# Kernel tuning notes

Measured on AMD Instinct MI355X. Metric: run time of the kernel, lower is better.

Reference implementation:

```python
import jax, jax.numpy as jnp
import numpy as np

N = 100000   # nodes
E = 1600000  # edges
D = 128      # in_dim == hidden_dim (residual-friendly)
C = 47       # num_classes
EPS = 1e-5   # BatchNorm eps


def _glorot(key, shape):
    fan = shape[0] + shape[1]
    return jax.random.uniform(key, shape, jnp.float32, -1.0, 1.0) * np.sqrt(6.0 / fan)


def setup_inputs() -> dict:
    key = jax.random.key(0)
    ks = jax.random.split(key, 16)
    inp = {
        "x": jax.random.normal(ks[0], (N, D), jnp.float32),
        "edge_index": jax.random.randint(ks[1], (2, E), 0, N, jnp.int32),
    }
    # Per-layer SAGEConv params: lin_l (root, with bias) and lin_r (neighbor, no bias)
    for i, k in zip((1, 2, 3), (ks[2], ks[3], ks[4])):
        k1, k2 = jax.random.split(k)
        inp[f"Wl{i}"] = _glorot(k1, (D, D))
        inp[f"bl{i}"] = jnp.zeros((D,), jnp.float32)
        inp[f"Wr{i}"] = _glorot(k2, (D, D))
        inp[f"bn_g{i}"] = jnp.ones((D,), jnp.float32)
        inp[f"bn_b{i}"] = jnp.zeros((D,), jnp.float32)
    inp["lin_W"] = _glorot(ks[5], (C, D))
    inp["lin_b"] = jnp.zeros((C,), jnp.float32)
    return inp


def _sage_conv(x, src, dst, Wl, bl, Wr):
    # mean aggregation of source features at destination nodes
    msg = jax.ops.segment_sum(x[src], dst, num_segments=N)            # [N, D]
    cnt = jax.ops.segment_sum(jnp.ones((src.shape[0],), x.dtype), dst, num_segments=N)
    mean = msg / jnp.maximum(cnt, 1.0)[:, None]
    return x @ Wl.T + bl + mean @ Wr.T


def _batch_norm(h, g, b):
    mu = h.mean(axis=0)
    var = h.var(axis=0)
    return (h - mu) * jax.lax.rsqrt(var + EPS) * g + b


def reference(x, edge_index,
              Wl1, bl1, Wr1, bn_g1, bn_b1,
              Wl2, bl2, Wr2, bn_g2, bn_b2,
              Wl3, bl3, Wr3, bn_g3, bn_b3,
              lin_W, lin_b):
    src, dst = edge_index[0], edge_index[1]
    layers = [(Wl1, bl1, Wr1, bn_g1, bn_b1),
              (Wl2, bl2, Wr2, bn_g2, bn_b2),
              (Wl3, bl3, Wr3, bn_g3, bn_b3)]
    for Wl, bl, Wr, g, b in layers:
        h = _sage_conv(x, src, dst, Wl, bl, Wr)
        h = jax.nn.relu(_batch_norm(h, g, b))
        # dropout is identity in deterministic/eval reference
        x = x + h  # shapes always match since in_dim == hidden_dim
    return x @ lin_W.T + lin_b
```

## Files before the change

kernel.cpp:

```cpp
#include <hip/hip_runtime.h>

typedef __attribute__((ext_vector_type(8))) short short8;
typedef __attribute__((ext_vector_type(4))) float f32x4;
typedef __attribute__((ext_vector_type(2))) float f32x2;

constexpr int NN = 100000;
constexpr int EE = 1600000;
constexpr int DD = 128;
constexpr int CC = 47;
constexpr int NB = 391;
constexpr int BSLOT = 5120;
constexpr int GB = 782;

constexpr size_t OFF_XB   = 0;
constexpr size_t OFF_MB   = 25600000;
constexpr size_t OFF_HB   = 51200000;
constexpr size_t OFF_XQ   = 76800000;
constexpr size_t OFF_BIN  = 89600000;
constexpr size_t OFF_CSR  = 97607680;
constexpr size_t OFF_RP   = 104007680;
constexpr size_t OFF_CUR  = 104407808;
constexpr size_t OFF_BASE = 104409856;
constexpr size_t OFF_W    = 104411904;
constexpr size_t OFF_ST   = 104620800;
constexpr size_t OFF_PB   = 104621824;

static __device__ __forceinline__ float bf2f(unsigned short u) {
    return __uint_as_float(((unsigned)u) << 16);
}
static __device__ __forceinline__ unsigned short f2bf(float f) {
    unsigned u = __float_as_uint(f);
    unsigned r = (u + 0x7fffu + ((u >> 16) & 1u)) >> 16;
    return (unsigned short)r;
}
static __device__ __forceinline__ uint2 pack8_fp8(const float* f) {
    int w0 = 0, w1 = 0;
    w0 = __builtin_amdgcn_cvt_pk_fp8_f32(f[0], f[1], w0, false);
    w0 = __builtin_amdgcn_cvt_pk_fp8_f32(f[2], f[3], w0, true);
    w1 = __builtin_amdgcn_cvt_pk_fp8_f32(f[4], f[5], w1, false);
    w1 = __builtin_amdgcn_cvt_pk_fp8_f32(f[6], f[7], w1, true);
    return uint2{(unsigned)w0, (unsigned)w1};
}

__global__ void k_convw(const float* __restrict__ wl1, const float* __restrict__ wr1,
                        const float* __restrict__ wl2, const float* __restrict__ wr2,
                        const float* __restrict__ wl3, const float* __restrict__ wr3,
                        const float* __restrict__ lw, unsigned short* __restrict__ dst) {
    int id = blockIdx.x * 256 + threadIdx.x;
    if (id < 98304) {
        int L = id >> 15;
        int r = id & 32767;
        int mat = r >> 14;
        int t = r & 16383;
        int j = t & 7, lane = (t >> 3) & 63, ct = (t >> 9) & 7, ks = t >> 12;
        int row = ct * 16 + (lane & 15);
        int col = ks * 32 + ((lane >> 4) << 3) + j;
        const float* src = (L == 0) ? (mat ? wr1 : wl1)
                         : (L == 1) ? (mat ? wr2 : wl2)
                                    : (mat ? wr3 : wl3);
        dst[id] = f2bf(src[row * 128 + col]);
    } else if (id < 98304 + 6144) {
        int t = id - 98304;
        int j = t & 7, lane = (t >> 3) & 63, m = t >> 9;
        int ct = m % 3, ks = m / 3;
        int row = ct * 16 + (lane & 15);
        int col = ks * 32 + ((lane >> 4) << 3) + j;
        dst[id] = (row < CC) ? f2bf(lw[row * 128 + col]) : (unsigned short)0;
    }
}

__global__ void k_convx(const float* __restrict__ x, unsigned short* __restrict__ xb,
                        unsigned char* __restrict__ xq) {
    int i = (blockIdx.x * 256 + threadIdx.x) * 8;
    if (i >= NN * DD) return;
    float4 v1 = *(const float4*)(x + i);
    float4 v2 = *(const float4*)(x + i + 4);
    float f[8] = {v1.x, v1.y, v1.z, v1.w, v2.x, v2.y, v2.z, v2.w};
    short8 o;
    #pragma unroll
    for (int j = 0; j < 8; ++j) o[j] = (short)f2bf(f[j]);
    *(short8*)(xb + i) = o;
    *(uint2*)(xq + i) = pack8_fp8(f);
}

__global__ __launch_bounds__(256) void k_bin(const int* __restrict__ ei,
                                             int* __restrict__ cur, int* __restrict__ bin) {
    __shared__ int cnt[NB];
    int t = threadIdx.x;
    for (int b = t; b < NB; b += 256) cnt[b] = 0;
    __syncthreads();
    int start = blockIdx.x * 3125;
    for (int i = t; i < 3125; i += 256) {
        int d = ei[EE + start + i];
        atomicAdd(&cnt[d >> 8], 1);
    }
    __syncthreads();
    int c[2], b0[2];
    #pragma unroll
    for (int k = 0; k < 2; ++k) {
        int b = t + k * 256;
        if (b < NB) { c[k] = cnt[b]; b0[k] = (c[k] > 0) ? atomicAdd(&cur[b], c[k]) : 0; }
    }
    __syncthreads();
    #pragma unroll
    for (int k = 0; k < 2; ++k) {
        int b = t + k * 256;
        if (b < NB) cnt[b] = b0[k];
    }
    __syncthreads();
    for (int i = t; i < 3125; i += 256) {
        int s = ei[start + i];
        int d = ei[EE + start + i];
        int b = d >> 8;
        int p = atomicAdd(&cnt[b], 1);
        if (p < BSLOT) bin[b * BSLOT + p] = (s << 8) | (d & 255);
    }
}

__global__ void k_base(const int* __restrict__ cur, int* __restrict__ base, int* __restrict__ rp) {
    __shared__ int sd[512];
    int t = threadIdx.x;
    int v0 = (t < NB) ? cur[t] : 0;
    sd[t] = v0;
    __syncthreads();
    for (int off = 1; off < 512; off <<= 1) {
        int v = (t >= off) ? sd[t - off] : 0;
        __syncthreads();
        sd[t] += v;
        __syncthreads();
    }
    if (t < NB) base[t] = sd[t] - v0;
    if (t == NB - 1) rp[NN] = sd[t];
}

__global__ __launch_bounds__(256) void k_build(const int* __restrict__ cur, const int* __restrict__ base,
                                               int* __restrict__ rp, const int* __restrict__ bin,
                                               int* __restrict__ csr) {
    __shared__ int lcnt[256], lsc[256], lrun[256];
    int b = blockIdx.x, t = threadIdx.x;
    int n0 = b << 8;
    int nodes = NN - n0; if (nodes > 256) nodes = 256;
    int tot = cur[b]; if (tot > BSLOT) tot = BSLOT;
    int bb = base[b];
    lcnt[t] = 0;
    __syncthreads();
    const int* bsrc = bin + b * BSLOT;
    for (int i = t; i < tot; i += 256) atomicAdd(&lcnt[bsrc[i] & 255], 1);
    __syncthreads();
    int c = lcnt[t];
    lsc[t] = c;
    __syncthreads();
    for (int off = 1; off < 256; off <<= 1) {
        int v = (t >= off) ? lsc[t - off] : 0;
        __syncthreads();
        lsc[t] += v;
        __syncthreads();
    }
    int excl = lsc[t] - c;
    if (t < nodes) rp[n0 + t] = bb + excl;
    lrun[t] = bb + excl;
    __syncthreads();
    for (int i = t; i < tot; i += 256) {
        int v = bsrc[i];
        int p = atomicAdd(&lrun[v & 255], 1);
        csr[p] = (v >> 8) << 7;
    }
}

__global__ __launch_bounds__(256) void k_agg(const int* __restrict__ rp, const int* __restrict__ csr,
                                             const unsigned char* __restrict__ xq,
                                             unsigned short* __restrict__ mb) {
    int node = blockIdx.x * 4 + (threadIdx.x >> 6);
    if (node >= NN) return;
    int lane = threadIdx.x & 63;
    int g = lane >> 4;
    int cb = (lane & 15) << 3;
    int s0 = rp[node], s1 = rp[node + 1];
    int deg = s1 - s0;
    f32x2 acc0 = {0.f, 0.f}, acc1 = {0.f, 0.f}, acc2 = {0.f, 0.f}, acc3 = {0.f, 0.f};
    int nb = deg >> 4;
    int e = s0 + g;
    for (int k = 0; k < nb; ++k) {
        int i0 = csr[e];
        int i1 = csr[e + 4];
        int i2 = csr[e + 8];
        int i3 = csr[e + 12];
        uint2 v0 = *(const uint2*)(xq + i0 + cb);
        uint2 v1 = *(const uint2*)(xq + i1 + cb);
        uint2 v2 = *(const uint2*)(xq + i2 + cb);
        uint2 v3 = *(const uint2*)(xq + i3 + cb);
        acc0 += __builtin_amdgcn_cvt_pk_f32_fp8(v0.x, false);
        acc1 += __builtin_amdgcn_cvt_pk_f32_fp8(v0.x, true);
        acc2 += __builtin_amdgcn_cvt_pk_f32_fp8(v0.y, false);
        acc3 += __builtin_amdgcn_cvt_pk_f32_fp8(v0.y, true);
        acc0 += __builtin_amdgcn_cvt_pk_f32_fp8(v1.x, false);
        acc1 += __builtin_amdgcn_cvt_pk_f32_fp8(v1.x, true);
        acc2 += __builtin_amdgcn_cvt_pk_f32_fp8(v1.y, false);
        acc3 += __builtin_amdgcn_cvt_pk_f32_fp8(v1.y, true);
        acc0 += __builtin_amdgcn_cvt_pk_f32_fp8(v2.x, false);
        acc1 += __builtin_amdgcn_cvt_pk_f32_fp8(v2.x, true);
        acc2 += __builtin_amdgcn_cvt_pk_f32_fp8(v2.y, false);
        acc3 += __builtin_amdgcn_cvt_pk_f32_fp8(v2.y, true);
        acc0 += __builtin_amdgcn_cvt_pk_f32_fp8(v3.x, false);
        acc1 += __builtin_amdgcn_cvt_pk_f32_fp8(v3.x, true);
        acc2 += __builtin_amdgcn_cvt_pk_f32_fp8(v3.y, false);
        acc3 += __builtin_amdgcn_cvt_pk_f32_fp8(v3.y, true);
        e += 16;
    }
    for (; e < s1; e += 4) {
        int i0 = csr[e];
        uint2 v0 = *(const uint2*)(xq + i0 + cb);
        acc0 += __builtin_amdgcn_cvt_pk_f32_fp8(v0.x, false);
        acc1 += __builtin_amdgcn_cvt_pk_f32_fp8(v0.x, true);
        acc2 += __builtin_amdgcn_cvt_pk_f32_fp8(v0.y, false);
        acc3 += __builtin_amdgcn_cvt_pk_f32_fp8(v0.y, true);
    }
    float acc[8] = {acc0[0], acc0[1], acc1[0], acc1[1],
                    acc2[0], acc2[1], acc3[0], acc3[1]};
    #pragma unroll
    for (int j = 0; j < 8; ++j) {
        acc[j] += __shfl_xor(acc[j], 16);
        acc[j] += __shfl_xor(acc[j], 32);
    }
    if (g == 0) {
        float inv = 1.0f / (float)(deg > 1 ? deg : 1);
        short8 o;
        #pragma unroll
        for (int j = 0; j < 8; ++j) o[j] = (short)f2bf(acc[j] * inv);
        *(short8*)(mb + (size_t)node * 128 + cb) = o;
    }
}

__global__ __launch_bounds__(256, 4) void k_gemm(const unsigned short* __restrict__ xb,
                                                 const unsigned short* __restrict__ mb,
                                                 const unsigned short* __restrict__ wf,
                                                 const float* __restrict__ bias,
                                                 unsigned short* __restrict__ hb,
                                                 float* __restrict__ pbuf) {
    __shared__ unsigned short wsh[16384];
    __shared__ float rbuf[1024];
    int tid = threadIdx.x;
    int wave = tid >> 6, lane = tid & 63, q = lane >> 4, l15 = lane & 15;
    int rowbase = blockIdx.x * 128 + wave * 32;

    f32x4 acc[2][8];
    #pragma unroll
    for (int ct = 0; ct < 8; ++ct) {
        float bv = bias[ct * 16 + l15];
        f32x4 t = {bv, bv, bv, bv};
        acc[0][ct] = t; acc[1][ct] = t;
    }

    #pragma unroll
    for (int mat = 0; mat < 2; ++mat) {
        const unsigned short* src = mat ? mb : xb;
        const int4* wsrc = (const int4*)(wf + (mat << 14));
        if (mat) __syncthreads();
        #pragma unroll
        for (int i = 0; i < 8; ++i)
            ((int4*)wsh)[tid + i * 256] = wsrc[tid + i * 256];
        __syncthreads();
        #pragma unroll
        for (int ks = 0; ks < 4; ++ks) {
            short8 a[2];
            #pragma unroll
            for (int rt = 0; rt < 2; ++rt) {
                int row = rowbase + rt * 16 + l15;
                if (row < NN) a[rt] = *(const short8*)(src + (size_t)row * 128 + ks * 32 + (q << 3));
                else          a[rt] = short8{0,0,0,0,0,0,0,0};
            }
            #pragma unroll
            for (int ct = 0; ct < 8; ++ct) {
                short8 b = *(const short8*)(wsh + ((ks * 8 + ct) << 9) + (lane << 3));
                acc[0][ct] = __builtin_amdgcn_mfma_f32_16x16x32_bf16(a[0], b, acc[0][ct], 0, 0, 0);
                acc[1][ct] = __builtin_amdgcn_mfma_f32_16x16x32_bf16(a[1], b, acc[1][ct], 0, 0, 0);
            }
        }
    }

    #pragma unroll
    for (int ct = 0; ct < 8; ++ct) {
        int colg = ct * 16 + l15;
        float sv = 0.f, qv = 0.f;
        #pragma unroll
        for (int rt = 0; rt < 2; ++rt) {
            #pragma unroll
            for (int r = 0; r < 4; ++r) {
                int row = rowbase + rt * 16 + (q << 2) + r;
                if (row < NN) {
                    float v = acc[rt][ct][r];
                    hb[(size_t)row * 128 + colg] = f2bf(v);
                    sv += v; qv += v * v;
                }
            }
        }
        sv += __shfl_xor(sv, 16); sv += __shfl_xor(sv, 32);
        qv += __shfl_xor(qv, 16); qv += __shfl_xor(qv, 32);
        if (q == 0) {
            rbuf[wave * 256 + colg] = sv;
            rbuf[wave * 256 + 128 + colg] = qv;
        }
    }
    __syncthreads();
    if (tid < 256) {
        float v = rbuf[tid] + rbuf[256 + tid] + rbuf[512 + tid] + rbuf[768 + tid];
        pbuf[(size_t)blockIdx.x * 256 + tid] = v;
    }
}

__global__ void k_stat2(const float* __restrict__ pbuf, float* __restrict__ st) {
    __shared__ float red[256];
    int b = blockIdx.x, t = threadIdx.x;
    int col = b * 32 + (t & 31);
    int rchunk = t >> 5;
    float s = 0.f;
    for (int r = rchunk; r < GB; r += 8) s += pbuf[(size_t)r * 256 + col];
    red[t] = s;
    __syncthreads();
    if (t < 32) {
        float v = 0.f;
        #pragma unroll
        for (int k = 0; k < 8; ++k) v += red[k * 32 + t];
        st[col] = v;
    }
}

__global__ void k_bn(const unsigned short* __restrict__ hb,
                     const float* __restrict__ stats, const float* __restrict__ gam,
                     const float* __restrict__ bet, unsigned short* __restrict__ xb,
                     unsigned char* __restrict__ xq) {
    int i = (blockIdx.x * 256 + threadIdx.x) * 8;
    if (i >= NN * DD) return;
    int col = i & 127;
    const float invN = 1.0f / (float)NN;
    short8 hv = *(const short8*)(hb + i);
    short8 xv = *(const short8*)(xb + i);
    short8 o;
    float f[8];
    #pragma unroll
    for (int j = 0; j < 8; ++j) {
        int c = col + j;
        float mu = stats[c] * invN;
        float var = stats[128 + c] * invN - mu * mu;
        float sc = rsqrtf(var + 1e-5f) * gam[c];
        float val = (bf2f((unsigned short)hv[j]) - mu) * sc + bet[c];
        float r = bf2f((unsigned short)xv[j]) + (val > 0.f ? val : 0.f);
        f[j] = r;
        o[j] = (short)f2bf(r);
    }
    *(short8*)(xb + i) = o;
    *(uint2*)(xq + i) = pack8_fp8(f);
}

__global__ __launch_bounds__(256) void k_final(const unsigned short* __restrict__ xb,
                                               const unsigned short* __restrict__ wf,
                                               const float* __restrict__ bias,
                                               float* __restrict__ out) {
    __shared__ unsigned short wsh[6144];
    int tid = threadIdx.x;
    #pragma unroll
    for (int i = 0; i < 3; ++i) {
        int idx = tid + i * 256;
        if (idx < 768) ((int4*)wsh)[idx] = ((const int4*)wf)[idx];
    }
    __syncthreads();

    int wave = tid >> 6, lane = tid & 63, q = lane >> 4, l15 = lane & 15;
    int rowbase = blockIdx.x * 256 + wave * 64;

    f32x4 acc[4][3];
    #pragma unroll
    for (int ct = 0; ct < 3; ++ct) {
        int colg = ct * 16 + l15;
        float bv = (colg < CC) ? bias[colg] : 0.f;
        f32x4 t = {bv, bv, bv, bv};
        #pragma unroll
        for (int rt = 0; rt < 4; ++rt) acc[rt][ct] = t;
    }
    #pragma unroll
    for (int ks = 0; ks < 4; ++ks) {
        short8 a[4];
        #pragma unroll
        for (int rt = 0; rt < 4; ++rt) {
            int row = rowbase + rt * 16 + l15;
            if (row < NN) a[rt] = *(const short8*)(xb + (size_t)row * 128 + ks * 32 + (q << 3));
            else          a[rt] = short8{0,0,0,0,0,0,0,0};
        }
        #pragma unroll
        for (int ct = 0; ct < 3; ++ct) {
            short8 b = *(const short8*)(wsh + ((ks * 3 + ct) << 9) + (lane << 3));
            #pragma unroll
            for (int rt = 0; rt < 4; ++rt)
                acc[rt][ct] = __builtin_amdgcn_mfma_f32_16x16x32_bf16(a[rt], b, acc[rt][ct], 0, 0, 0);
        }
    }
    #pragma unroll
    for (int ct = 0; ct < 3; ++ct) {
        int colg = ct * 16 + l15;
        if (colg >= CC) continue;
        #pragma unroll
        for (int rt = 0; rt < 4; ++rt) {
            #pragma unroll
            for (int r = 0; r < 4; ++r) {
                int row = rowbase + rt * 16 + (q << 2) + r;
                if (row < NN) out[(size_t)row * CC + colg] = acc[rt][ct][r];
            }
        }
    }
}

extern "C" void kernel_launch(void* const* d_in, const int* in_sizes, int n_in,
                              void* d_out, int out_size, void* d_ws, size_t ws_size,
                              hipStream_t stream) {
    const float* x   = (const float*)d_in[0];
    const int*   ei  = (const int*)d_in[1];
    const float* Wl[3]  = {(const float*)d_in[2],  (const float*)d_in[7],  (const float*)d_in[12]};
    const float* bl[3]  = {(const float*)d_in[3],  (const float*)d_in[8],  (const float*)d_in[13]};
    const float* Wr[3]  = {(const float*)d_in[4],  (const float*)d_in[9],  (const float*)d_in[14]};
    const float* bng[3] = {(const float*)d_in[5],  (const float*)d_in[10], (const float*)d_in[15]};
    const float* bnb[3] = {(const float*)d_in[6],  (const float*)d_in[11], (const float*)d_in[16]};
    const float* linW = (const float*)d_in[17];
    const float* linb = (const float*)d_in[18];

    char* ws = (char*)d_ws;
    unsigned short* xb   = (unsigned short*)(ws + OFF_XB);
    unsigned short* mb   = (unsigned short*)(ws + OFF_MB);
    unsigned short* hb   = (unsigned short*)(ws + OFF_HB);
    unsigned char*  xq   = (unsigned char*)(ws + OFF_XQ);
    int*            bin  = (int*)(ws + OFF_BIN);
    int*            csr  = (int*)(ws + OFF_CSR);
    int*            rp   = (int*)(ws + OFF_RP);
    int*            cur  = (int*)(ws + OFF_CUR);
    int*            base = (int*)(ws + OFF_BASE);
    unsigned short* wfr  = (unsigned short*)(ws + OFF_W);
    float*          st   = (float*)(ws + OFF_ST);
    float*          pbuf = (float*)(ws + OFF_PB);

    hipMemsetAsync(cur, 0, (size_t)NB * 4, stream);
    k_convw<<<408, 256, 0, stream>>>(Wl[0], Wr[0], Wl[1], Wr[1], Wl[2], Wr[2], linW, wfr);
    k_convx<<<6250, 256, 0, stream>>>(x, xb, xq);
    k_bin<<<512, 256, 0, stream>>>(ei, cur, bin);
    k_base<<<1, 512, 0, stream>>>(cur, base, rp);
    k_build<<<NB, 256, 0, stream>>>(cur, base, rp, bin, csr);

    for (int l = 0; l < 3; ++l) {
        k_agg<<<25000, 256, 0, stream>>>(rp, csr, xq, mb);
        k_gemm<<<GB, 256, 0, stream>>>(xb, mb, wfr + (size_t)l * 32768, bl[l], hb, pbuf);
        k_stat2<<<8, 256, 0, stream>>>(pbuf, st);
        k_bn<<<6250, 256, 0, stream>>>(hb, st, bng[l], bnb[l], xb, xq);
    }
    k_final<<<391, 256, 0, stream>>>(xb, wfr + 98304, linb, (float*)d_out);
}
```

Baseline: 532.2 us.

## Fuse neighbor aggregation into GEMM kernel via shared-memory mean tile

```diff
diff --git a/kernel.cpp b/kernel.cpp
--- a/kernel.cpp
+++ b/kernel.cpp
@@ -167,82 +167,84 @@
     }
 }
 
-__global__ __launch_bounds__(256) void k_agg(const int* __restrict__ rp, const int* __restrict__ csr,
-                                             const unsigned char* __restrict__ xq,
-                                             unsigned short* __restrict__ mb) {
-    int node = blockIdx.x * 4 + (threadIdx.x >> 6);
-    if (node >= NN) return;
-    int lane = threadIdx.x & 63;
-    int g = lane >> 4;
-    int cb = (lane & 15) << 3;
-    int s0 = rp[node], s1 = rp[node + 1];
-    int deg = s1 - s0;
-    f32x2 acc0 = {0.f, 0.f}, acc1 = {0.f, 0.f}, acc2 = {0.f, 0.f}, acc3 = {0.f, 0.f};
-    int nb = deg >> 4;
-    int e = s0 + g;
-    for (int k = 0; k < nb; ++k) {
-        int i0 = csr[e];
-        int i1 = csr[e + 4];
-        int i2 = csr[e + 8];
-        int i3 = csr[e + 12];
-        uint2 v0 = *(const uint2*)(xq + i0 + cb);
-        uint2 v1 = *(const uint2*)(xq + i1 + cb);
-        uint2 v2 = *(const uint2*)(xq + i2 + cb);
-        uint2 v3 = *(const uint2*)(xq + i3 + cb);
-        acc0 += __builtin_amdgcn_cvt_pk_f32_fp8(v0.x, false);
-        acc1 += __builtin_amdgcn_cvt_pk_f32_fp8(v0.x, true);
-        acc2 += __builtin_amdgcn_cvt_pk_f32_fp8(v0.y, false);
-        acc3 += __builtin_amdgcn_cvt_pk_f32_fp8(v0.y, true);
-        acc0 += __builtin_amdgcn_cvt_pk_f32_fp8(v1.x, false);
-        acc1 += __builtin_amdgcn_cvt_pk_f32_fp8(v1.x, true);
-        acc2 += __builtin_amdgcn_cvt_pk_f32_fp8(v1.y, false);
-        acc3 += __builtin_amdgcn_cvt_pk_f32_fp8(v1.y, true);
-        acc0 += __builtin_amdgcn_cvt_pk_f32_fp8(v2.x, false);
-        acc1 += __builtin_amdgcn_cvt_pk_f32_fp8(v2.x, true);
-        acc2 += __builtin_amdgcn_cvt_pk_f32_fp8(v2.y, false);
-        acc3 += __builtin_amdgcn_cvt_pk_f32_fp8(v2.y, true);
-        acc0 += __builtin_amdgcn_cvt_pk_f32_fp8(v3.x, false);
-        acc1 += __builtin_amdgcn_cvt_pk_f32_fp8(v3.x, true);
-        acc2 += __builtin_amdgcn_cvt_pk_f32_fp8(v3.y, false);
-        acc3 += __builtin_amdgcn_cvt_pk_f32_fp8(v3.y, true);
-        e += 16;
-    }
-    for (; e < s1; e += 4) {
-        int i0 = csr[e];
-        uint2 v0 = *(const uint2*)(xq + i0 + cb);
-        acc0 += __builtin_amdgcn_cvt_pk_f32_fp8(v0.x, false);
-        acc1 += __builtin_amdgcn_cvt_pk_f32_fp8(v0.x, true);
-        acc2 += __builtin_amdgcn_cvt_pk_f32_fp8(v0.y, false);
-        acc3 += __builtin_amdgcn_cvt_pk_f32_fp8(v0.y, true);
-    }
-    float acc[8] = {acc0[0], acc0[1], acc1[0], acc1[1],
-                    acc2[0], acc2[1], acc3[0], acc3[1]};
-    #pragma unroll
-    for (int j = 0; j < 8; ++j) {
-        acc[j] += __shfl_xor(acc[j], 16);
-        acc[j] += __shfl_xor(acc[j], 32);
-    }
-    if (g == 0) {
-        float inv = 1.0f / (float)(deg > 1 ? deg : 1);
-        short8 o;
-        #pragma unroll
-        for (int j = 0; j < 8; ++j) o[j] = (short)f2bf(acc[j] * inv);
-        *(short8*)(mb + (size_t)node * 128 + cb) = o;
-    }
-}
-
-__global__ __launch_bounds__(256, 4) void k_gemm(const unsigned short* __restrict__ xb,
-                                                 const unsigned short* __restrict__ mb,
-                                                 const unsigned short* __restrict__ wf,
-                                                 const float* __restrict__ bias,
-                                                 unsigned short* __restrict__ hb,
-                                                 float* __restrict__ pbuf) {
-    __shared__ unsigned short wsh[16384];
+__global__ __launch_bounds__(256, 4) void k_fused(const int* __restrict__ rp,
+                                                  const int* __restrict__ csr,
+                                                  const unsigned char* __restrict__ xq,
+                                                  const unsigned short* __restrict__ xb,
+                                                  const unsigned short* __restrict__ wf,
+                                                  const float* __restrict__ bias,
+                                                  unsigned short* __restrict__ hb,
+                                                  float* __restrict__ pbuf) {
+    __shared__ unsigned short msh[16384];
     __shared__ float rbuf[1024];
     int tid = threadIdx.x;
     int wave = tid >> 6, lane = tid & 63, q = lane >> 4, l15 = lane & 15;
     int rowbase = blockIdx.x * 128 + wave * 32;
 
+    int g = q;
+    int cb = l15 << 3;
+    #pragma unroll 1
+    for (int i = 0; i < 32; ++i) {
+        int node = rowbase + i;
+        if (node >= NN) break;
+        int s0 = rp[node], s1 = rp[node + 1];
+        int deg = s1 - s0;
+        f32x2 a0 = {0.f, 0.f}, a1 = {0.f, 0.f}, a2 = {0.f, 0.f}, a3 = {0.f, 0.f};
+        int nbt = deg >> 4;
+        int e = s0 + g;
+        for (int k = 0; k < nbt; ++k) {
+            int i0 = csr[e];
+            int i1 = csr[e + 4];
+            int i2 = csr[e + 8];
+            int i3 = csr[e + 12];
+            uint2 v0 = *(const uint2*)(xq + i0 + cb);
+            uint2 v1 = *(const uint2*)(xq + i1 + cb);
+            uint2 v2 = *(const uint2*)(xq + i2 + cb);
+            uint2 v3 = *(const uint2*)(xq + i3 + cb);
+            a0 += __builtin_amdgcn_cvt_pk_f32_fp8(v0.x, false);
+            a1 += __builtin_amdgcn_cvt_pk_f32_fp8(v0.x, true);
+            a2 += __builtin_amdgcn_cvt_pk_f32_fp8(v0.y, false);
+            a3 += __builtin_amdgcn_cvt_pk_f32_fp8(v0.y, true);
+            a0 += __builtin_amdgcn_cvt_pk_f32_fp8(v1.x, false);
+            a1 += __builtin_amdgcn_cvt_pk_f32_fp8(v1.x, true);
+            a2 += __builtin_amdgcn_cvt_pk_f32_fp8(v1.y, false);
+            a3 += __builtin_amdgcn_cvt_pk_f32_fp8(v1.y, true);
+            a0 += __builtin_amdgcn_cvt_pk_f32_fp8(v2.x, false);
+            a1 += __builtin_amdgcn_cvt_pk_f32_fp8(v2.x, true);
+            a2 += __builtin_amdgcn_cvt_pk_f32_fp8(v2.y, false);
+            a3 += __builtin_amdgcn_cvt_pk_f32_fp8(v2.y, true);
+            a0 += __builtin_amdgcn_cvt_pk_f32_fp8(v3.x, false);
+            a1 += __builtin_amdgcn_cvt_pk_f32_fp8(v3.x, true);
+            a2 += __builtin_amdgcn_cvt_pk_f32_fp8(v3.y, false);
+            a3 += __builtin_amdgcn_cvt_pk_f32_fp8(v3.y, true);
+            e += 16;
+        }
+        for (; e < s1; e += 4) {
+            int i0 = csr[e];
+            uint2 v0 = *(const uint2*)(xq + i0 + cb);
+            a0 += __builtin_amdgcn_cvt_pk_f32_fp8(v0.x, false);
+            a1 += __builtin_amdgcn_cvt_pk_f32_fp8(v0.x, true);
+            a2 += __builtin_amdgcn_cvt_pk_f32_fp8(v0.y, false);
+            a3 += __builtin_amdgcn_cvt_pk_f32_fp8(v0.y, true);
+        }
+        float acc[8] = {a0[0], a0[1], a1[0], a1[1], a2[0], a2[1], a3[0], a3[1]};
+        #pragma unroll
+        for (int j = 0; j < 8; ++j) {
+            acc[j] += __shfl_xor(acc[j], 16);
+            acc[j] += __shfl_xor(acc[j], 32);
+        }
+        if (g == 0) {
+            float inv = 1.0f / (float)(deg > 1 ? deg : 1);
+            short8 o;
+            #pragma unroll
+            for (int j = 0; j < 8; ++j) o[j] = (short)f2bf(acc[j] * inv);
+            int brow = wave * 32 + i;
+            int byt = (cb << 1) ^ ((brow & 15) << 4);
+            *(short8*)((unsigned char*)msh + brow * 256 + byt) = o;
+        }
+    }
+    __syncthreads();
+
     f32x4 acc[2][8];
     #pragma unroll
     for (int ct = 0; ct < 8; ++ct) {
@@ -252,29 +254,35 @@
     }
 
     #pragma unroll
-    for (int mat = 0; mat < 2; ++mat) {
-        const unsigned short* src = mat ? mb : xb;
-        const int4* wsrc = (const int4*)(wf + (mat << 14));
-        if (mat) __syncthreads();
-        #pragma unroll
-        for (int i = 0; i < 8; ++i)
-            ((int4*)wsh)[tid + i * 256] = wsrc[tid + i * 256];
-        __syncthreads();
-        #pragma unroll
-        for (int ks = 0; ks < 4; ++ks) {
-            short8 a[2];
-            #pragma unroll
-            for (int rt = 0; rt < 2; ++rt) {
-                int row = rowbase + rt * 16 + l15;
-                if (row < NN) a[rt] = *(const short8*)(src + (size_t)row * 128 + ks * 32 + (q << 3));
-                else          a[rt] = short8{0,0,0,0,0,0,0,0};
-            }
-            #pragma unroll
-            for (int ct = 0; ct < 8; ++ct) {
-                short8 b = *(const short8*)(wsh + ((ks * 8 + ct) << 9) + (lane << 3));
-                acc[0][ct] = __builtin_amdgcn_mfma_f32_16x16x32_bf16(a[0], b, acc[0][ct], 0, 0, 0);
-                acc[1][ct] = __builtin_amdgcn_mfma_f32_16x16x32_bf16(a[1], b, acc[1][ct], 0, 0, 0);
-            }
+    for (int ks = 0; ks < 4; ++ks) {
+        short8 a[2];
+        #pragma unroll
+        for (int rt = 0; rt < 2; ++rt) {
+            int row = rowbase + rt * 16 + l15;
+            if (row < NN) a[rt] = *(const short8*)(xb + (size_t)row * 128 + ks * 32 + (q << 3));
+            else          a[rt] = short8{0,0,0,0,0,0,0,0};
+        }
+        #pragma unroll
+        for (int ct = 0; ct < 8; ++ct) {
+            short8 b = *(const short8*)(wf + ((ks * 8 + ct) << 9) + (lane << 3));
+            acc[0][ct] = __builtin_amdgcn_mfma_f32_16x16x32_bf16(a[0], b, acc[0][ct], 0, 0, 0);
+            acc[1][ct] = __builtin_amdgcn_mfma_f32_16x16x32_bf16(a[1], b, acc[1][ct], 0, 0, 0);
+        }
+    }
+    #pragma unroll
+    for (int ks = 0; ks < 4; ++ks) {
+        short8 a[2];
+        #pragma unroll
+        for (int rt = 0; rt < 2; ++rt) {
+            int lr = wave * 32 + rt * 16 + l15;
+            int byt = ((ks << 6) + (q << 4)) ^ (l15 << 4);
+            a[rt] = *(const short8*)((const unsigned char*)msh + lr * 256 + byt);
+        }
+        #pragma unroll
+        for (int ct = 0; ct < 8; ++ct) {
+            short8 b = *(const short8*)(wf + 16384 + ((ks * 8 + ct) << 9) + (lane << 3));
+            acc[0][ct] = __builtin_amdgcn_mfma_f32_16x16x32_bf16(a[0], b, acc[0][ct], 0, 0, 0);
+            acc[1][ct] = __builtin_amdgcn_mfma_f32_16x16x32_bf16(a[1], b, acc[1][ct], 0, 0, 0);
         }
     }
 
@@ -424,7 +432,6 @@
 
     char* ws = (char*)d_ws;
     unsigned short* xb   = (unsigned short*)(ws + OFF_XB);
-    unsigned short* mb   = (unsigned short*)(ws + OFF_MB);
     unsigned short* hb   = (unsigned short*)(ws + OFF_HB);
     unsigned char*  xq   = (unsigned char*)(ws + OFF_XQ);
     int*            bin  = (int*)(ws + OFF_BIN);
@@ -444,8 +451,7 @@
     k_build<<<NB, 256, 0, stream>>>(cur, base, rp, bin, csr);
 
     for (int l = 0; l < 3; ++l) {
-        k_agg<<<25000, 256, 0, stream>>>(rp, csr, xq, mb);
-        k_gemm<<<GB, 256, 0, stream>>>(xb, mb, wfr + (size_t)l * 32768, bl[l], hb, pbuf);
+        k_fused<<<GB, 256, 0, stream>>>(rp, csr, xq, xb, wfr + (size_t)l * 32768, bl[l], hb, pbuf);
         k_stat2<<<8, 256, 0, stream>>>(pbuf, st);
         k_bn<<<6250, 256, 0, stream>>>(hb, st, bng[l], bnb[l], xb, xq);
     }
```

Measured after the change: 632.0 us. 1.19x slower.

## Overlap root-weight GEMM with neighbor aggregation by interleaving blocks in one kernel

Applied to the files above, without the earlier changes.

```diff
diff --git a/kernel.cpp b/kernel.cpp
--- a/kernel.cpp
+++ b/kernel.cpp
@@ -3,6 +3,7 @@
 typedef __attribute__((ext_vector_type(8))) short short8;
 typedef __attribute__((ext_vector_type(4))) float f32x4;
 typedef __attribute__((ext_vector_type(2))) float f32x2;
+typedef __attribute__((ext_vector_type(4))) int i32x4;
 
 constexpr int NN = 100000;
 constexpr int EE = 1600000;
@@ -11,6 +12,8 @@
 constexpr int NB = 391;
 constexpr int BSLOT = 5120;
 constexpr int GB = 782;
+constexpr int GL = 1563;
+constexpr int GA2 = 26563;
 
 constexpr size_t OFF_XB   = 0;
 constexpr size_t OFF_MB   = 25600000;
@@ -167,14 +170,65 @@
     }
 }
 
-__global__ __launch_bounds__(256) void k_agg(const int* __restrict__ rp, const int* __restrict__ csr,
-                                             const unsigned char* __restrict__ xq,
-                                             unsigned short* __restrict__ mb) {
-    int node = blockIdx.x * 4 + (threadIdx.x >> 6);
+__global__ __launch_bounds__(256, 6) void k_agg2(const int* __restrict__ rp,
+                                                 const int* __restrict__ csr,
+                                                 const unsigned char* __restrict__ xq,
+                                                 unsigned short* __restrict__ mb,
+                                                 const unsigned short* __restrict__ xb,
+                                                 const unsigned short* __restrict__ wf,
+                                                 const float* __restrict__ bias,
+                                                 unsigned short* __restrict__ hb) {
+    int gid = blockIdx.x;
+    int tid = threadIdx.x;
+    int lane = tid & 63, q = (lane >> 4), l15 = lane & 15;
+
+    if (gid % 17 == 0) {
+        int gl = gid / 17;
+        int wave = tid >> 6;
+        int rowbase = gl * 64 + wave * 16;
+        f32x4 acc[8];
+        #pragma unroll
+        for (int ct = 0; ct < 8; ++ct) {
+            float bv = bias[ct * 16 + l15];
+            f32x4 t = {bv, bv, bv, bv};
+            acc[ct] = t;
+        }
+        #pragma unroll
+        for (int ks = 0; ks < 4; ++ks) {
+            int row = rowbase + l15;
+            short8 a;
+            if (row < NN) {
+                i32x4 av = __builtin_nontemporal_load(
+                    (const i32x4*)(xb + (size_t)row * 128 + ks * 32 + (q << 3)));
+                a = *(short8*)&av;
+            } else {
+                a = short8{0,0,0,0,0,0,0,0};
+            }
+            #pragma unroll
+            for (int ct = 0; ct < 8; ++ct) {
+                short8 b = *(const short8*)(wf + ((ks * 8 + ct) << 9) + (lane << 3));
+                acc[ct] = __builtin_amdgcn_mfma_f32_16x16x32_bf16(a, b, acc[ct], 0, 0, 0);
+            }
+        }
+        #pragma unroll
+        for (int ct = 0; ct < 8; ++ct) {
+            int colg = ct * 16 + l15;
+            #pragma unroll
+            for (int r = 0; r < 4; ++r) {
+                int row = rowbase + (q << 2) + r;
+                if (row < NN)
+                    __builtin_nontemporal_store(f2bf(acc[ct][r]),
+                                                hb + (size_t)row * 128 + colg);
+            }
+        }
+        return;
+    }
+
+    int ai = gid - gid / 17 - 1;
+    int node = ai * 4 + (tid >> 6);
     if (node >= NN) return;
-    int lane = threadIdx.x & 63;
-    int g = lane >> 4;
-    int cb = (lane & 15) << 3;
+    int g = q;
+    int cb = l15 << 3;
     int s0 = rp[node], s1 = rp[node + 1];
     int deg = s1 - s0;
     f32x2 acc0 = {0.f, 0.f}, acc1 = {0.f, 0.f}, acc2 = {0.f, 0.f}, acc3 = {0.f, 0.f};
@@ -231,50 +285,42 @@
     }
 }
 
-__global__ __launch_bounds__(256, 4) void k_gemm(const unsigned short* __restrict__ xb,
-                                                 const unsigned short* __restrict__ mb,
-                                                 const unsigned short* __restrict__ wf,
-                                                 const float* __restrict__ bias,
-                                                 unsigned short* __restrict__ hb,
-                                                 float* __restrict__ pbuf) {
+__global__ __launch_bounds__(256, 4) void k_gemmR(const unsigned short* __restrict__ mb,
+                                                  const unsigned short* __restrict__ wf,
+                                                  unsigned short* __restrict__ hb,
+                                                  float* __restrict__ pbuf) {
     __shared__ unsigned short wsh[16384];
     __shared__ float rbuf[1024];
     int tid = threadIdx.x;
     int wave = tid >> 6, lane = tid & 63, q = lane >> 4, l15 = lane & 15;
     int rowbase = blockIdx.x * 128 + wave * 32;
 
+    const int4* wsrc = (const int4*)(wf + 16384);
+    #pragma unroll
+    for (int i = 0; i < 8; ++i)
+        ((int4*)wsh)[tid + i * 256] = wsrc[tid + i * 256];
+    __syncthreads();
+
     f32x4 acc[2][8];
     #pragma unroll
     for (int ct = 0; ct < 8; ++ct) {
-        float bv = bias[ct * 16 + l15];
-        f32x4 t = {bv, bv, bv, bv};
-        acc[0][ct] = t; acc[1][ct] = t;
-    }
-
-    #pragma unroll
-    for (int mat = 0; mat < 2; ++mat) {
-        const unsigned short* src = mat ? mb : xb;
-        const int4* wsrc = (const int4*)(wf + (mat << 14));
-        if (mat) __syncthreads();
-        #pragma unroll
-        for (int i = 0; i < 8; ++i)
-            ((int4*)wsh)[tid + i * 256] = wsrc[tid + i * 256];
-        __syncthreads();
-        #pragma unroll
-        for (int ks = 0; ks < 4; ++ks) {
-            short8 a[2];
-            #pragma unroll
-            for (int rt = 0; rt < 2; ++rt) {
-                int row = rowbase + rt * 16 + l15;
-                if (row < NN) a[rt] = *(const short8*)(src + (size_t)row * 128 + ks * 32 + (q << 3));
-                else          a[rt] = short8{0,0,0,0,0,0,0,0};
-            }
-            #pragma unroll
-            for (int ct = 0; ct < 8; ++ct) {
-                short8 b = *(const short8*)(wsh + ((ks * 8 + ct) << 9) + (lane << 3));
-                acc[0][ct] = __builtin_amdgcn_mfma_f32_16x16x32_bf16(a[0], b, acc[0][ct], 0, 0, 0);
-                acc[1][ct] = __builtin_amdgcn_mfma_f32_16x16x32_bf16(a[1], b, acc[1][ct], 0, 0, 0);
-            }
+        f32x4 z = {0.f, 0.f, 0.f, 0.f};
+        acc[0][ct] = z; acc[1][ct] = z;
+    }
+    #pragma unroll
+    for (int ks = 0; ks < 4; ++ks) {
+        short8 a[2];
+        #pragma unroll
+        for (int rt = 0; rt < 2; ++rt) {
+            int row = rowbase + rt * 16 + l15;
+            if (row < NN) a[rt] = *(const short8*)(mb + (size_t)row * 128 + ks * 32 + (q << 3));
+            else          a[rt] = short8{0,0,0,0,0,0,0,0};
+        }
+        #pragma unroll
+        for (int ct = 0; ct < 8; ++ct) {
+            short8 b = *(const short8*)(wsh + ((ks * 8 + ct) << 9) + (lane << 3));
+            acc[0][ct] = __builtin_amdgcn_mfma_f32_16x16x32_bf16(a[0], b, acc[0][ct], 0, 0, 0);
+            acc[1][ct] = __builtin_amdgcn_mfma_f32_16x16x32_bf16(a[1], b, acc[1][ct], 0, 0, 0);
         }
     }
 
@@ -288,8 +334,9 @@
             for (int r = 0; r < 4; ++r) {
                 int row = rowbase + rt * 16 + (q << 2) + r;
                 if (row < NN) {
-                    float v = acc[rt][ct][r];
-                    hb[(size_t)row * 128 + colg] = f2bf(v);
+                    size_t idx = (size_t)row * 128 + colg;
+                    float v = acc[rt][ct][r] + bf2f(hb[idx]);
+                    hb[idx] = f2bf(v);
                     sv += v; qv += v * v;
                 }
             }
@@ -444,8 +491,9 @@
     k_build<<<NB, 256, 0, stream>>>(cur, base, rp, bin, csr);
 
     for (int l = 0; l < 3; ++l) {
-        k_agg<<<25000, 256, 0, stream>>>(rp, csr, xq, mb);
-        k_gemm<<<GB, 256, 0, stream>>>(xb, mb, wfr + (size_t)l * 32768, bl[l], hb, pbuf);
+        const unsigned short* wfp = wfr + (size_t)l * 32768;
+        k_agg2<<<GA2, 256, 0, stream>>>(rp, csr, xq, mb, xb, wfp, bl[l], hb);
+        k_gemmR<<<GB, 256, 0, stream>>>(mb, wfp, hb, pbuf);
         k_stat2<<<8, 256, 0, stream>>>(pbuf, st);
         k_bn<<<6250, 256, 0, stream>>>(hb, st, bng[l], bnb[l], xb, xq);
     }
```

Result: slower. 632.3 us (+18.8%).

## Merge prep kernels, fold bin prefix into build, atomically reduce BN stats

Applied to the files above, without the earlier changes.

```diff
diff --git a/kernel.cpp b/kernel.cpp
--- a/kernel.cpp
+++ b/kernel.cpp
@@ -23,7 +23,6 @@
 constexpr size_t OFF_BASE = 104409856;
 constexpr size_t OFF_W    = 104411904;
 constexpr size_t OFF_ST   = 104620800;
-constexpr size_t OFF_PB   = 104621824;
 
 static __device__ __forceinline__ float bf2f(unsigned short u) {
     return __uint_as_float(((unsigned)u) << 16);
@@ -42,45 +41,48 @@
     return uint2{(unsigned)w0, (unsigned)w1};
 }
 
-__global__ void k_convw(const float* __restrict__ wl1, const float* __restrict__ wr1,
-                        const float* __restrict__ wl2, const float* __restrict__ wr2,
-                        const float* __restrict__ wl3, const float* __restrict__ wr3,
-                        const float* __restrict__ lw, unsigned short* __restrict__ dst) {
-    int id = blockIdx.x * 256 + threadIdx.x;
-    if (id < 98304) {
-        int L = id >> 15;
-        int r = id & 32767;
-        int mat = r >> 14;
-        int t = r & 16383;
-        int j = t & 7, lane = (t >> 3) & 63, ct = (t >> 9) & 7, ks = t >> 12;
-        int row = ct * 16 + (lane & 15);
-        int col = ks * 32 + ((lane >> 4) << 3) + j;
-        const float* src = (L == 0) ? (mat ? wr1 : wl1)
-                         : (L == 1) ? (mat ? wr2 : wl2)
-                                    : (mat ? wr3 : wl3);
-        dst[id] = f2bf(src[row * 128 + col]);
-    } else if (id < 98304 + 6144) {
-        int t = id - 98304;
-        int j = t & 7, lane = (t >> 3) & 63, m = t >> 9;
-        int ct = m % 3, ks = m / 3;
-        int row = ct * 16 + (lane & 15);
-        int col = ks * 32 + ((lane >> 4) << 3) + j;
-        dst[id] = (row < CC) ? f2bf(lw[row * 128 + col]) : (unsigned short)0;
-    }
-}
-
-__global__ void k_convx(const float* __restrict__ x, unsigned short* __restrict__ xb,
-                        unsigned char* __restrict__ xq) {
-    int i = (blockIdx.x * 256 + threadIdx.x) * 8;
-    if (i >= NN * DD) return;
-    float4 v1 = *(const float4*)(x + i);
-    float4 v2 = *(const float4*)(x + i + 4);
-    float f[8] = {v1.x, v1.y, v1.z, v1.w, v2.x, v2.y, v2.z, v2.w};
-    short8 o;
-    #pragma unroll
-    for (int j = 0; j < 8; ++j) o[j] = (short)f2bf(f[j]);
-    *(short8*)(xb + i) = o;
-    *(uint2*)(xq + i) = pack8_fp8(f);
+__global__ void k_prep(const float* __restrict__ wl1, const float* __restrict__ wr1,
+                       const float* __restrict__ wl2, const float* __restrict__ wr2,
+                       const float* __restrict__ wl3, const float* __restrict__ wr3,
+                       const float* __restrict__ lw, unsigned short* __restrict__ wdst,
+                       const float* __restrict__ x, unsigned short* __restrict__ xb,
+                       unsigned char* __restrict__ xq, int* __restrict__ cur) {
+    int bid = blockIdx.x;
+    int id = bid * 256 + threadIdx.x;
+    if (id < NB) cur[id] = 0;
+    if (bid < 408) {
+        if (id < 98304) {
+            int L = id >> 15;
+            int r = id & 32767;
+            int mat = r >> 14;
+            int t = r & 16383;
+            int j = t & 7, lane = (t >> 3) & 63, ct = (t >> 9) & 7, ks = t >> 12;
+            int row = ct * 16 + (lane & 15);
+            int col = ks * 32 + ((lane >> 4) << 3) + j;
+            const float* src = (L == 0) ? (mat ? wr1 : wl1)
+                             : (L == 1) ? (mat ? wr2 : wl2)
+                                        : (mat ? wr3 : wl3);
+            wdst[id] = f2bf(src[row * 128 + col]);
+        } else if (id < 98304 + 6144) {
+            int t = id - 98304;
+            int j = t & 7, lane = (t >> 3) & 63, m = t >> 9;
+            int ct = m % 3, ks = m / 3;
+            int row = ct * 16 + (lane & 15);
+            int col = ks * 32 + ((lane >> 4) << 3) + j;
+            wdst[id] = (row < CC) ? f2bf(lw[row * 128 + col]) : (unsigned short)0;
+        }
+    } else {
+        int i = ((bid - 408) * 256 + threadIdx.x) * 8;
+        if (i >= NN * DD) return;
+        float4 v1 = *(const float4*)(x + i);
+        float4 v2 = *(const float4*)(x + i + 4);
+        float f[8] = {v1.x, v1.y, v1.z, v1.w, v2.x, v2.y, v2.z, v2.w};
+        short8 o;
+        #pragma unroll
+        for (int j = 0; j < 8; ++j) o[j] = (short)f2bf(f[j]);
+        *(short8*)(xb + i) = o;
+        *(uint2*)(xq + i) = pack8_fp8(f);
+    }
 }
 
 __global__ __launch_bounds__(256) void k_bin(const int* __restrict__ ei,
@@ -117,31 +119,26 @@
     }
 }
 
-__global__ void k_base(const int* __restrict__ cur, int* __restrict__ base, int* __restrict__ rp) {
-    __shared__ int sd[512];
-    int t = threadIdx.x;
-    int v0 = (t < NB) ? cur[t] : 0;
-    sd[t] = v0;
-    __syncthreads();
-    for (int off = 1; off < 512; off <<= 1) {
-        int v = (t >= off) ? sd[t - off] : 0;
-        __syncthreads();
-        sd[t] += v;
-        __syncthreads();
-    }
-    if (t < NB) base[t] = sd[t] - v0;
-    if (t == NB - 1) rp[NN] = sd[t];
-}
-
-__global__ __launch_bounds__(256) void k_build(const int* __restrict__ cur, const int* __restrict__ base,
+__global__ __launch_bounds__(256) void k_build(const int* __restrict__ cur,
                                                int* __restrict__ rp, const int* __restrict__ bin,
                                                int* __restrict__ csr) {
-    __shared__ int lcnt[256], lsc[256], lrun[256];
+    __shared__ int lcnt[256], lsc[256], lrun[256], red[256];
     int b = blockIdx.x, t = threadIdx.x;
+    int partial = 0;
+    for (int i = t; i < b; i += 256) partial += cur[i];
+    red[t] = partial;
+    __syncthreads();
+    for (int off = 128; off > 0; off >>= 1) {
+        if (t < off) red[t] += red[t + off];
+        __syncthreads();
+    }
+    int bb = red[0];
+    __syncthreads();
+    if (b == NB - 1 && t == 0) rp[NN] = bb + cur[b];
+
     int n0 = b << 8;
     int nodes = NN - n0; if (nodes > 256) nodes = 256;
     int tot = cur[b]; if (tot > BSLOT) tot = BSLOT;
-    int bb = base[b];
     lcnt[t] = 0;
     __syncthreads();
     const int* bsrc = bin + b * BSLOT;
@@ -169,7 +166,9 @@
 
 __global__ __launch_bounds__(256) void k_agg(const int* __restrict__ rp, const int* __restrict__ csr,
                                              const unsigned char* __restrict__ xq,
-                                             unsigned short* __restrict__ mb) {
+                                             unsigned short* __restrict__ mb,
+                                             float* __restrict__ st) {
+    if (blockIdx.x == 0) st[threadIdx.x] = 0.f;
     int node = blockIdx.x * 4 + (threadIdx.x >> 6);
     if (node >= NN) return;
     int lane = threadIdx.x & 63;
@@ -236,7 +235,7 @@
                                                  const unsigned short* __restrict__ wf,
                                                  const float* __restrict__ bias,
                                                  unsigned short* __restrict__ hb,
-                                                 float* __restrict__ pbuf) {
+                                                 float* __restrict__ st) {
     __shared__ unsigned short wsh[16384];
     __shared__ float rbuf[1024];
     int tid = threadIdx.x;
@@ -304,24 +303,7 @@
     __syncthreads();
     if (tid < 256) {
         float v = rbuf[tid] + rbuf[256 + tid] + rbuf[512 + tid] + rbuf[768 + tid];
-        pbuf[(size_t)blockIdx.x * 256 + tid] = v;
-    }
-}
-
-__global__ void k_stat2(const float* __restrict__ pbuf, float* __restrict__ st) {
-    __shared__ float red[256];
-    int b = blockIdx.x, t = threadIdx.x;
-    int col = b * 32 + (t & 31);
-    int rchunk = t >> 5;
-    float s = 0.f;
-    for (int r = rchunk; r < GB; r += 8) s += pbuf[(size_t)r * 256 + col];
-    red[t] = s;
-    __syncthreads();
-    if (t < 32) {
-        float v = 0.f;
-        #pragma unroll
-        for (int k = 0; k < 8; ++k) v += red[k * 32 + t];
-        st[col] = v;
+        atomicAdd(&st[tid], v);
     }
 }
 
@@ -431,22 +413,18 @@
     int*            csr  = (int*)(ws + OFF_CSR);
     int*            rp   = (int*)(ws + OFF_RP);
     int*            cur  = (int*)(ws + OFF_CUR);
-    int*            base = (int*)(ws + OFF_BASE);
     unsigned short* wfr  = (unsigned short*)(ws + OFF_W);
     float*          st   = (float*)(ws + OFF_ST);
-    float*          pbuf = (float*)(ws + OFF_PB);
-
-    hipMemsetAsync(cur, 0, (size_t)NB * 4, stream);
-    k_convw<<<408, 256, 0, stream>>>(Wl[0], Wr[0], Wl[1], Wr[1], Wl[2], Wr[2], linW, wfr);
-    k_convx<<<6250, 256, 0, stream>>>(x, xb, xq);
+
+    k_prep<<<6658, 256, 0, stream>>>(Wl[0], Wr[0], Wl[1], Wr[1], Wl[2], Wr[2], linW, wfr,
+                                     x, xb, xq, cur);
     k_bin<<<512, 256, 0, stream>>>(ei, cur, bin);
-    k_base<<<1, 512, 0, stream>>>(cur, base, rp);
-    k_build<<<NB, 256, 0, stream>>>(cur, base, rp, bin, csr);
+    k_build<<<NB, 256, 0, stream>>>(cur, rp, bin, csr);
 
     for (int l = 0; l < 3; ++l) {
-        k_agg<<<25000, 256, 0, stream>>>(rp, csr, xq, mb);
-        k_gemm<<<GB, 256, 0, stream>>>(xb, mb, wfr + (size_t)l * 32768, bl[l], hb, pbuf);
-        k_stat2<<<8, 256, 0, stream>>>(pbuf, st);
+        const unsigned short* wfp = wfr + (size_t)l * 32768;
+        k_agg<<<25000, 256, 0, stream>>>(rp, csr, xq, mb, st);
+        k_gemm<<<GB, 256, 0, stream>>>(xb, mb, wfp, bl[l], hb, st);
         k_bn<<<6250, 256, 0, stream>>>(hb, st, bng[l], bnb[l], xb, xq);
     }
     k_final<<<391, 256, 0, stream>>>(xb, wfr + 98304, linb, (float*)d_out);
```

Result: faster. 484.4 us (-9.0%).
